# Kernel optimization log

Measured on AMD Instinct MI355X. Metric: run time of the kernel, lower is better.

The kernel has to match this reference:

```python
import jax, jax.numpy as jnp
import numpy as np

NUM_EXPERTS = 128
INPUT_DIM = 128
HIDDEN_DIM = 512
OUTPUT_DIM = 128
TOKENS_PER_EXPERT = 2048


def make_identity_experts(num_experts, input_dim, output_dim):
    # identical to the torch helper: zeros with ones on the (square) diagonal
    d = min(input_dim, output_dim)
    w = jnp.zeros((num_experts, input_dim, output_dim), dtype=jnp.float32)
    idx = jnp.arange(d)
    return w.at[:, idx, idx].set(1.0)


def setup_inputs() -> dict:
    key = jax.random.key(0)
    k_tok, = jax.random.split(key, 1)
    group_token = jax.random.normal(
        k_tok, (NUM_EXPERTS, TOKENS_PER_EXPERT, INPUT_DIM), dtype=jnp.float32)
    weights1 = make_identity_experts(NUM_EXPERTS, INPUT_DIM, HIDDEN_DIM)
    weights2 = make_identity_experts(NUM_EXPERTS, HIDDEN_DIM, OUTPUT_DIM)
    return {"group_token": group_token, "weights1": weights1, "weights2": weights2}


def reference(group_token, weights1, weights2):
    # grouped GEMM 1: per-expert [T, in] @ [in, hid]
    h = jnp.einsum('etd,edh->eth', group_token, weights1)
    # exact (erf-based) GELU, matching torch.nn.functional.gelu default
    h = jax.nn.gelu(h, approximate=False)
    # grouped GEMM 2: per-expert [T, hid] @ [hid, out]
    out = jnp.einsum('eth,eho->eto', h, weights2)
    return out
```

## Files before the change

kernel.cpp:

```cpp
#include <hip/hip_runtime.h>
#include <hip/hip_bf16.h>
#include <stdint.h>

typedef __attribute__((ext_vector_type(8))) short s8v;
typedef __attribute__((ext_vector_type(4))) float f4v;
typedef __attribute__((ext_vector_type(4))) int i4v;

#define NE   128
#define NT   2048
#define DIN  128
#define DH   512
#define DOUT 128

__device__ __forceinline__ ushort f2bf(float f) {
  uint32_t u = __float_as_uint(f);
  u += 0x7FFFu + ((u >> 16) & 1u);
  return (ushort)(u >> 16);
}

__device__ __forceinline__ float gelu_f(float x) {
  float t = 0.7978845608028654f * x * (1.0f + 0.044715f * x * x);
  float e = __expf(2.0f * t);
  float th = (e - 1.0f) / (e + 1.0f);
  return 0.5f * x * (1.0f + th);
}

__global__ __launch_bounds__(256) void transpose_cvt(
    const float* __restrict__ src, ushort* __restrict__ dst, int R, int C) {
  const int tilesR = R >> 6, tilesC = C >> 6;
  const int bid = blockIdx.x;
  const int e   = bid / (tilesR * tilesC);
  const int rem = bid % (tilesR * tilesC);
  const int tr = rem / tilesC, tc = rem % tilesC;
  const float* S = src + (size_t)e * R * C + (size_t)(tr << 6) * C + (tc << 6);
  ushort*      D = dst + (size_t)e * R * C + (size_t)(tc << 6) * R + (tr << 6);
  __shared__ float tile[64][65];
  const int tid = threadIdx.x;
#pragma unroll
  for (int it = 0; it < 4; ++it) {
    int s = (it << 8) + tid;
    int r = s >> 4, cg = (s & 15) << 2;
    float4 v = *(const float4*)(S + (size_t)r * C + cg);
    tile[r][cg + 0] = v.x; tile[r][cg + 1] = v.y;
    tile[r][cg + 2] = v.z; tile[r][cg + 3] = v.w;
  }
  __syncthreads();
#pragma unroll
  for (int it = 0; it < 4; ++it) {
    int s = (it << 8) + tid;
    int c = s >> 4, rg = (s & 15) << 2;
    ushort4 w;
    w.x = f2bf(tile[rg + 0][c]); w.y = f2bf(tile[rg + 1][c]);
    w.z = f2bf(tile[rg + 2][c]); w.w = f2bf(tile[rg + 3][c]);
    *(ushort4*)(D + (size_t)c * R + rg) = w;
  }
}

__global__ __launch_bounds__(256, 2) void moe_fused(
    const float* __restrict__ X, const ushort* __restrict__ W1t,
    const ushort* __restrict__ W2t, float* __restrict__ Out) {
  __shared__ ushort Xs[128 * 128];
  __shared__ ushort W1s[32 * 128];
  __shared__ ushort W2s[128 * 32];
  __shared__ ushort Hs[128 * 32];

  const int tid  = threadIdx.x;
  const int lane = tid & 63;
  const int wid  = tid >> 6;
  const int quad = lane >> 4;
  const int l16  = lane & 15;

  const int e    = blockIdx.x >> 4;
  const int tile = blockIdx.x & 15;

  const float*  Xe  = X   + ((size_t)e * NT + (size_t)tile * 128) * DIN;
  const ushort* W1e = W1t + (size_t)e * DH * DIN;
  const ushort* W2e = W2t + (size_t)e * DOUT * DH;
  float*        Oe  = Out + ((size_t)e * NT + (size_t)tile * 128) * DOUT;

#pragma unroll
  for (int it = 0; it < 8; ++it) {
    int s = (it << 8) + tid;
    int m = s >> 4, c = s & 15;
    const float* p = Xe + m * DIN + (c << 3);
    float4 v0 = *(const float4*)p;
    float4 v1 = *(const float4*)(p + 4);
    s8v w;
    w[0] = (short)f2bf(v0.x); w[1] = (short)f2bf(v0.y);
    w[2] = (short)f2bf(v0.z); w[3] = (short)f2bf(v0.w);
    w[4] = (short)f2bf(v1.x); w[5] = (short)f2bf(v1.y);
    w[6] = (short)f2bf(v1.z); w[7] = (short)f2bf(v1.w);
    *(s8v*)(Xs + (m << 7) + ((c ^ (m & 15)) << 3)) = w;
  }

  const f4v zero4 = {0.0f, 0.0f, 0.0f, 0.0f};
  f4v oacc[4][4];
#pragma unroll
  for (int i = 0; i < 4; ++i)
#pragma unroll
    for (int j = 0; j < 4; ++j) oacc[i][j] = zero4;

  const int w_h  = (wid >> 1) << 4;
  const int w_m1 = (wid & 1) << 6;
  const int w_m2 = (wid >> 1) << 6;
  const int w_o  = (wid & 1) << 6;

  for (int ch = 0; ch < 16; ++ch) {
    const int h0 = ch << 5;
    __syncthreads();
#pragma unroll
    for (int it = 0; it < 2; ++it) {
      int s = (it << 8) + tid;
      int r = s >> 4, c = s & 15;
      i4v v = *(const i4v*)(W1e + (size_t)(h0 + r) * DIN + (c << 3));
      *(i4v*)(W1s + (r << 7) + ((c ^ (r & 15)) << 3)) = v;
    }
#pragma unroll
    for (int it = 0; it < 2; ++it) {
      int s = (it << 8) + tid;
      int r = s >> 2, c = s & 3;
      i4v v = *(const i4v*)(W2e + (size_t)r * DH + h0 + (c << 3));
      *(i4v*)(W2s + (r << 5) + ((c ^ ((r >> 1) & 3)) << 3)) = v;
    }
    __syncthreads();

    f4v hacc[4];
    hacc[0] = zero4; hacc[1] = zero4; hacc[2] = zero4; hacc[3] = zero4;
#pragma unroll
    for (int ks = 0; ks < 4; ++ks) {
      int hl = w_h + l16;
      int ca = (ks << 2) + quad;
      s8v af = *(const s8v*)(W1s + (hl << 7) + ((ca ^ (hl & 15)) << 3));
#pragma unroll
      for (int mt = 0; mt < 4; ++mt) {
        int m = w_m1 + (mt << 4) + l16;
        s8v bf = *(const s8v*)(Xs + (m << 7) + ((ca ^ (m & 15)) << 3));
        hacc[mt] = __builtin_amdgcn_mfma_f32_16x16x32_bf16(af, bf, hacc[mt], 0, 0, 0);
      }
    }
#pragma unroll
    for (int mt = 0; mt < 4; ++mt) {
      int m  = w_m1 + (mt << 4) + l16;
      int hq = w_h + (quad << 2);
      ushort4 w;
      w.x = f2bf(gelu_f(hacc[mt][0]));
      w.y = f2bf(gelu_f(hacc[mt][1]));
      w.z = f2bf(gelu_f(hacc[mt][2]));
      w.w = f2bf(gelu_f(hacc[mt][3]));
      int cc = hq >> 3, half = (hq >> 2) & 1;
      *(ushort4*)(Hs + (m << 5) + ((cc ^ ((m >> 1) & 3)) << 3) + (half << 2)) = w;
    }
    __syncthreads();

    s8v af2[4], bf2[4];
#pragma unroll
    for (int mt = 0; mt < 4; ++mt) {
      int m = w_m2 + (mt << 4) + l16;
      af2[mt] = *(const s8v*)(Hs + (m << 5) + ((quad ^ ((m >> 1) & 3)) << 3));
    }
#pragma unroll
    for (int ot = 0; ot < 4; ++ot) {
      int o = w_o + (ot << 4) + l16;
      bf2[ot] = *(const s8v*)(W2s + (o << 5) + ((quad ^ ((o >> 1) & 3)) << 3));
    }
#pragma unroll
    for (int mt = 0; mt < 4; ++mt)
#pragma unroll
      for (int ot = 0; ot < 4; ++ot)
        oacc[mt][ot] = __builtin_amdgcn_mfma_f32_16x16x32_bf16(af2[mt], bf2[ot], oacc[mt][ot], 0, 0, 0);
  }

#pragma unroll
  for (int mt = 0; mt < 4; ++mt) {
    int mb = w_m2 + (mt << 4) + (quad << 2);
#pragma unroll
    for (int ot = 0; ot < 4; ++ot) {
      int o = w_o + (ot << 4) + l16;
      float* q = Oe + (size_t)mb * DOUT + o;
      q[0 * DOUT] = oacc[mt][ot][0];
      q[1 * DOUT] = oacc[mt][ot][1];
      q[2 * DOUT] = oacc[mt][ot][2];
      q[3 * DOUT] = oacc[mt][ot][3];
    }
  }
}

extern "C" void kernel_launch(void* const* d_in, const int* in_sizes, int n_in,
                              void* d_out, int out_size, void* d_ws, size_t ws_size,
                              hipStream_t stream) {
  const float* X  = (const float*)d_in[0];
  const float* W1 = (const float*)d_in[1];
  const float* W2 = (const float*)d_in[2];
  float* Out = (float*)d_out;

  ushort* W1t = (ushort*)d_ws;
  ushort* W2t = (ushort*)d_ws + (size_t)NE * DH * DIN;

  transpose_cvt<<<NE * (DIN / 64) * (DH / 64), 256, 0, stream>>>(W1, W1t, DIN, DH);
  transpose_cvt<<<NE * (DH / 64) * (DOUT / 64), 256, 0, stream>>>(W2, W2t, DH, DOUT);
  moe_fused<<<NE * (NT / 128), 256, 0, stream>>>(X, W1t, W2t, Out);
}
```

Before: 387.2 us.

## Pre-pack weights into MFMA fragment order and keep X and H in registers

Replaces the transpose kernels with pack kernels that write W1 and W2 already laid out in per-lane MFMA fragment order. The fused kernel now holds X fragments and the GELU output in registers, feeding the second GEMM with 16x16x16 MFMA. This removes the Xs and Hs shared buffers and one barrier per chunk. Weight chunks are double-buffered through direct global-to-LDS loads, and occupancy is raised to 3 blocks per SM. GELU becomes a sigmoid-form tanh approximation using a fast reciprocal, which adds small numerical error relative to exact erf GELU.

```diff
diff --git a/kernel.cpp b/kernel.cpp
--- a/kernel.cpp
+++ b/kernel.cpp
@@ -3,8 +3,8 @@
 #include <stdint.h>
 
 typedef __attribute__((ext_vector_type(8))) short s8v;
+typedef __attribute__((ext_vector_type(4))) short s4v;
 typedef __attribute__((ext_vector_type(4))) float f4v;
-typedef __attribute__((ext_vector_type(4))) int i4v;
 
 #define NE   128
 #define NT   2048
@@ -12,175 +12,187 @@
 #define DH   512
 #define DOUT 128
 
-__device__ __forceinline__ ushort f2bf(float f) {
-  uint32_t u = __float_as_uint(f);
-  u += 0x7FFFu + ((u >> 16) & 1u);
-  return (ushort)(u >> 16);
+#define MFMA32(a,b,c) __builtin_amdgcn_mfma_f32_16x16x32_bf16(a,b,c,0,0,0)
+#define MFMA16(a,b,c) __builtin_amdgcn_mfma_f32_16x16x16bf16_1k(a,b,c,0,0,0)
+
+#define GLOAD16(g,l) __builtin_amdgcn_global_load_lds( \
+    (const __attribute__((address_space(1))) void*)(g), \
+    (__attribute__((address_space(3))) void*)(l), 16, 0, 0)
+
+__device__ __forceinline__ __hip_bfloat162 pk2(float a, float b) {
+  float2 t; t.x = a; t.y = b;
+  return __float22bfloat162_rn(t);
+}
+
+__device__ __forceinline__ s8v pack8(float4 a, float4 b) {
+  union { s8v v; __hip_bfloat162 h[4]; } u;
+  u.h[0] = pk2(a.x, a.y); u.h[1] = pk2(a.z, a.w);
+  u.h[2] = pk2(b.x, b.y); u.h[3] = pk2(b.z, b.w);
+  return u.v;
 }
 
 __device__ __forceinline__ float gelu_f(float x) {
-  float t = 0.7978845608028654f * x * (1.0f + 0.044715f * x * x);
-  float e = __expf(2.0f * t);
-  float th = (e - 1.0f) / (e + 1.0f);
-  return 0.5f * x * (1.0f + th);
-}
-
-__global__ __launch_bounds__(256) void transpose_cvt(
-    const float* __restrict__ src, ushort* __restrict__ dst, int R, int C) {
-  const int tilesR = R >> 6, tilesC = C >> 6;
-  const int bid = blockIdx.x;
-  const int e   = bid / (tilesR * tilesC);
-  const int rem = bid % (tilesR * tilesC);
-  const int tr = rem / tilesC, tc = rem % tilesC;
-  const float* S = src + (size_t)e * R * C + (size_t)(tr << 6) * C + (tc << 6);
-  ushort*      D = dst + (size_t)e * R * C + (size_t)(tc << 6) * R + (tr << 6);
-  __shared__ float tile[64][65];
+  float x2 = x * x;
+  float p  = __builtin_fmaf(x2, 0.07135481f, 1.5957691f);
+  float e  = __expf(-x * p);
+  return x * __builtin_amdgcn_rcpf(1.0f + e);
+}
+
+__global__ __launch_bounds__(256) void pack_w1(const float* __restrict__ W1,
+                                               ushort* __restrict__ W1F) {
+  const int e = blockIdx.x >> 4, t2 = blockIdx.x & 15;
+  __shared__ float T[128][36];
   const int tid = threadIdx.x;
-#pragma unroll
-  for (int it = 0; it < 4; ++it) {
-    int s = (it << 8) + tid;
-    int r = s >> 4, cg = (s & 15) << 2;
-    float4 v = *(const float4*)(S + (size_t)r * C + cg);
-    tile[r][cg + 0] = v.x; tile[r][cg + 1] = v.y;
-    tile[r][cg + 2] = v.z; tile[r][cg + 3] = v.w;
-  }
+  const int d = tid >> 1, half = tid & 1;
+  const float* src = W1 + (size_t)e * (DIN * DH) + (size_t)d * DH + t2 * 32 + half * 16;
+  float4 v0 = *(const float4*)src;
+  float4 v1 = *(const float4*)(src + 4);
+  float4 v2 = *(const float4*)(src + 8);
+  float4 v3 = *(const float4*)(src + 12);
+  float* trow = &T[d][half * 16];
+  *(float4*)(trow + 0) = v0; *(float4*)(trow + 4)  = v1;
+  *(float4*)(trow + 8) = v2; *(float4*)(trow + 12) = v3;
   __syncthreads();
-#pragma unroll
-  for (int it = 0; it < 4; ++it) {
-    int s = (it << 8) + tid;
-    int c = s >> 4, rg = (s & 15) << 2;
-    ushort4 w;
-    w.x = f2bf(tile[rg + 0][c]); w.y = f2bf(tile[rg + 1][c]);
-    w.z = f2bf(tile[rg + 2][c]); w.w = f2bf(tile[rg + 3][c]);
-    *(ushort4*)(D + (size_t)c * R + rg) = w;
-  }
-}
-
-__global__ __launch_bounds__(256, 2) void moe_fused(
-    const float* __restrict__ X, const ushort* __restrict__ W1t,
-    const ushort* __restrict__ W2t, float* __restrict__ Out) {
-  __shared__ ushort Xs[128 * 128];
-  __shared__ ushort W1s[32 * 128];
-  __shared__ ushort W2s[128 * 32];
-  __shared__ ushort Hs[128 * 32];
+  const int lane = tid & 63, ks = tid >> 6;
+  const int q = lane >> 4, l16 = lane & 15;
+#pragma unroll
+  for (int hl = 0; hl < 2; ++hl) {
+    float g[8];
+#pragma unroll
+    for (int j = 0; j < 8; ++j) g[j] = T[ks * 32 + q * 8 + j][hl * 16 + l16];
+    float4 a; a.x = g[0]; a.y = g[1]; a.z = g[2]; a.w = g[3];
+    float4 b; b.x = g[4]; b.y = g[5]; b.z = g[6]; b.w = g[7];
+    *(s8v*)(W1F + ((((size_t)e * 32 + t2 * 2 + hl) * 4) + ks) * 512 + lane * 8) = pack8(a, b);
+  }
+}
+
+__global__ __launch_bounds__(256) void pack_w2(const float* __restrict__ W2,
+                                               ushort* __restrict__ W2F) {
+  const int e = blockIdx.x >> 5, ht = blockIdx.x & 31;
+  __shared__ float T[16][132];
+  const int tid = threadIdx.x;
+  const int h = tid >> 4, c16 = tid & 15;
+  const float* src = W2 + (size_t)e * (DH * DOUT) + (size_t)(ht * 16 + h) * DOUT + c16 * 8;
+  float4 v0 = *(const float4*)src;
+  float4 v1 = *(const float4*)(src + 4);
+  float* trow = &T[h][c16 * 8];
+  *(float4*)(trow + 0) = v0; *(float4*)(trow + 4) = v1;
+  __syncthreads();
+  const int lane = tid & 63;
+  const int q = lane >> 4, l16 = lane & 15;
+#pragma unroll
+  for (int i = 0; i < 2; ++i) {
+    int ot = (tid >> 6) + i * 4;
+    float g0 = T[4 * q + 0][ot * 16 + l16];
+    float g1 = T[4 * q + 1][ot * 16 + l16];
+    float g2 = T[4 * q + 2][ot * 16 + l16];
+    float g3 = T[4 * q + 3][ot * 16 + l16];
+    union { s4v v; __hip_bfloat162 h2[2]; } u;
+    u.h2[0] = pk2(g0, g1); u.h2[1] = pk2(g2, g3);
+    *(s4v*)(W2F + (((size_t)e * 32 + ht) * 8 + ot) * 256 + lane * 4) = u.v;
+  }
+}
+
+__global__ __launch_bounds__(256, 3) void moe_fused(
+    const float* __restrict__ X, const ushort* __restrict__ W1F,
+    const ushort* __restrict__ W2F, float* __restrict__ Out) {
+  __shared__ __align__(16) ushort W1s[2][4096];
+  __shared__ __align__(16) ushort W2s[2][4096];
 
   const int tid  = threadIdx.x;
   const int lane = tid & 63;
   const int wid  = tid >> 6;
-  const int quad = lane >> 4;
+  const int q    = lane >> 4;
   const int l16  = lane & 15;
 
   const int e    = blockIdx.x >> 4;
   const int tile = blockIdx.x & 15;
 
-  const float*  Xe  = X   + ((size_t)e * NT + (size_t)tile * 128) * DIN;
-  const ushort* W1e = W1t + (size_t)e * DH * DIN;
-  const ushort* W2e = W2t + (size_t)e * DOUT * DH;
-  float*        Oe  = Out + ((size_t)e * NT + (size_t)tile * 128) * DOUT;
-
-#pragma unroll
-  for (int it = 0; it < 8; ++it) {
-    int s = (it << 8) + tid;
-    int m = s >> 4, c = s & 15;
-    const float* p = Xe + m * DIN + (c << 3);
-    float4 v0 = *(const float4*)p;
-    float4 v1 = *(const float4*)(p + 4);
-    s8v w;
-    w[0] = (short)f2bf(v0.x); w[1] = (short)f2bf(v0.y);
-    w[2] = (short)f2bf(v0.z); w[3] = (short)f2bf(v0.w);
-    w[4] = (short)f2bf(v1.x); w[5] = (short)f2bf(v1.y);
-    w[6] = (short)f2bf(v1.z); w[7] = (short)f2bf(v1.w);
-    *(s8v*)(Xs + (m << 7) + ((c ^ (m & 15)) << 3)) = w;
+  const float* Xe  = X + ((size_t)e * NT + (size_t)tile * 128) * DIN;
+  const ushort* W1e = W1F + (size_t)e * 65536;
+  const ushort* W2e = W2F + (size_t)e * 65536;
+  float* Oe = Out + ((size_t)e * NT + (size_t)tile * 128) * DOUT;
+
+  s8v xf[2][4];
+#pragma unroll
+  for (int mt = 0; mt < 2; ++mt) {
+#pragma unroll
+    for (int ks = 0; ks < 4; ++ks) {
+      const float* p = Xe + (size_t)(wid * 32 + mt * 16 + l16) * DIN + ks * 32 + q * 8;
+      float4 v0 = *(const float4*)p;
+      float4 v1 = *(const float4*)(p + 4);
+      xf[mt][ks] = pack8(v0, v1);
+    }
   }
 
   const f4v zero4 = {0.0f, 0.0f, 0.0f, 0.0f};
-  f4v oacc[4][4];
-#pragma unroll
-  for (int i = 0; i < 4; ++i)
-#pragma unroll
-    for (int j = 0; j < 4; ++j) oacc[i][j] = zero4;
-
-  const int w_h  = (wid >> 1) << 4;
-  const int w_m1 = (wid & 1) << 6;
-  const int w_m2 = (wid >> 1) << 6;
-  const int w_o  = (wid & 1) << 6;
-
-  for (int ch = 0; ch < 16; ++ch) {
-    const int h0 = ch << 5;
+  f4v oacc[2][8];
+#pragma unroll
+  for (int mt = 0; mt < 2; ++mt)
+#pragma unroll
+    for (int ot = 0; ot < 8; ++ot) oacc[mt][ot] = zero4;
+
+  {
+    const ushort* g1 = W1e;
+    const ushort* g2 = W2e;
+#pragma unroll
+    for (int i = 0; i < 2; ++i) {
+      int u = i * 256 + tid;
+      GLOAD16(g1 + u * 8, &W1s[0][u * 8]);
+      GLOAD16(g2 + u * 8, &W2s[0][u * 8]);
+    }
+  }
+  __syncthreads();
+
+  for (int c = 0; c < 16; ++c) {
+    const int buf = c & 1;
+    if (c < 15) {
+      const ushort* g1 = W1e + (c + 1) * 4096;
+      const ushort* g2 = W2e + (c + 1) * 4096;
+#pragma unroll
+      for (int i = 0; i < 2; ++i) {
+        int u = i * 256 + tid;
+        GLOAD16(g1 + u * 8, &W1s[buf ^ 1][u * 8]);
+        GLOAD16(g2 + u * 8, &W2s[buf ^ 1][u * 8]);
+      }
+    }
+#pragma unroll
+    for (int hl = 0; hl < 2; ++hl) {
+      f4v hacc[2]; hacc[0] = zero4; hacc[1] = zero4;
+#pragma unroll
+      for (int ks = 0; ks < 4; ++ks) {
+        s8v af = *(const s8v*)&W1s[buf][(hl * 4 + ks) * 512 + lane * 8];
+        hacc[0] = MFMA32(af, xf[0][ks], hacc[0]);
+        hacc[1] = MFMA32(af, xf[1][ks], hacc[1]);
+      }
+      s4v a2[2];
+#pragma unroll
+      for (int mt = 0; mt < 2; ++mt) {
+        union { s4v v; __hip_bfloat162 h2[2]; } u;
+        u.h2[0] = pk2(gelu_f(hacc[mt][0]), gelu_f(hacc[mt][1]));
+        u.h2[1] = pk2(gelu_f(hacc[mt][2]), gelu_f(hacc[mt][3]));
+        a2[mt] = u.v;
+      }
+#pragma unroll
+      for (int ot = 0; ot < 8; ++ot) {
+        s4v bf = *(const s4v*)&W2s[buf][(hl * 8 + ot) * 256 + lane * 4];
+        oacc[0][ot] = MFMA16(a2[0], bf, oacc[0][ot]);
+        oacc[1][ot] = MFMA16(a2[1], bf, oacc[1][ot]);
+      }
+    }
     __syncthreads();
-#pragma unroll
-    for (int it = 0; it < 2; ++it) {
-      int s = (it << 8) + tid;
-      int r = s >> 4, c = s & 15;
-      i4v v = *(const i4v*)(W1e + (size_t)(h0 + r) * DIN + (c << 3));
-      *(i4v*)(W1s + (r << 7) + ((c ^ (r & 15)) << 3)) = v;
-    }
-#pragma unroll
-    for (int it = 0; it < 2; ++it) {
-      int s = (it << 8) + tid;
-      int r = s >> 2, c = s & 3;
-      i4v v = *(const i4v*)(W2e + (size_t)r * DH + h0 + (c << 3));
-      *(i4v*)(W2s + (r << 5) + ((c ^ ((r >> 1) & 3)) << 3)) = v;
-    }
-    __syncthreads();
-
-    f4v hacc[4];
-    hacc[0] = zero4; hacc[1] = zero4; hacc[2] = zero4; hacc[3] = zero4;
-#pragma unroll
-    for (int ks = 0; ks < 4; ++ks) {
-      int hl = w_h + l16;
-      int ca = (ks << 2) + quad;
-      s8v af = *(const s8v*)(W1s + (hl << 7) + ((ca ^ (hl & 15)) << 3));
-#pragma unroll
-      for (int mt = 0; mt < 4; ++mt) {
-        int m = w_m1 + (mt << 4) + l16;
-        s8v bf = *(const s8v*)(Xs + (m << 7) + ((ca ^ (m & 15)) << 3));
-        hacc[mt] = __builtin_amdgcn_mfma_f32_16x16x32_bf16(af, bf, hacc[mt], 0, 0, 0);
-      }
-    }
-#pragma unroll
-    for (int mt = 0; mt < 4; ++mt) {
-      int m  = w_m1 + (mt << 4) + l16;
-      int hq = w_h + (quad << 2);
-      ushort4 w;
-      w.x = f2bf(gelu_f(hacc[mt][0]));
-      w.y = f2bf(gelu_f(hacc[mt][1]));
-      w.z = f2bf(gelu_f(hacc[mt][2]));
-      w.w = f2bf(gelu_f(hacc[mt][3]));
-      int cc = hq >> 3, half = (hq >> 2) & 1;
-      *(ushort4*)(Hs + (m << 5) + ((cc ^ ((m >> 1) & 3)) << 3) + (half << 2)) = w;
-    }
-    __syncthreads();
-
-    s8v af2[4], bf2[4];
-#pragma unroll
-    for (int mt = 0; mt < 4; ++mt) {
-      int m = w_m2 + (mt << 4) + l16;
-      af2[mt] = *(const s8v*)(Hs + (m << 5) + ((quad ^ ((m >> 1) & 3)) << 3));
-    }
-#pragma unroll
-    for (int ot = 0; ot < 4; ++ot) {
-      int o = w_o + (ot << 4) + l16;
-      bf2[ot] = *(const s8v*)(W2s + (o << 5) + ((quad ^ ((o >> 1) & 3)) << 3));
-    }
-#pragma unroll
-    for (int mt = 0; mt < 4; ++mt)
-#pragma unroll
-      for (int ot = 0; ot < 4; ++ot)
-        oacc[mt][ot] = __builtin_amdgcn_mfma_f32_16x16x32_bf16(af2[mt], bf2[ot], oacc[mt][ot], 0, 0, 0);
-  }
-
-#pragma unroll
-  for (int mt = 0; mt < 4; ++mt) {
-    int mb = w_m2 + (mt << 4) + (quad << 2);
-#pragma unroll
-    for (int ot = 0; ot < 4; ++ot) {
-      int o = w_o + (ot << 4) + l16;
-      float* q = Oe + (size_t)mb * DOUT + o;
-      q[0 * DOUT] = oacc[mt][ot][0];
-      q[1 * DOUT] = oacc[mt][ot][1];
-      q[2 * DOUT] = oacc[mt][ot][2];
-      q[3 * DOUT] = oacc[mt][ot][3];
+  }
+
+#pragma unroll
+  for (int mt = 0; mt < 2; ++mt) {
+    const int mb = wid * 32 + mt * 16 + 4 * q;
+#pragma unroll
+    for (int ot = 0; ot < 8; ++ot) {
+      float* p = Oe + (size_t)mb * DOUT + ot * 16 + l16;
+      p[0 * DOUT] = oacc[mt][ot][0];
+      p[1 * DOUT] = oacc[mt][ot][1];
+      p[2 * DOUT] = oacc[mt][ot][2];
+      p[3 * DOUT] = oacc[mt][ot][3];
     }
   }
 }
@@ -193,10 +205,10 @@
   const float* W2 = (const float*)d_in[2];
   float* Out = (float*)d_out;
 
-  ushort* W1t = (ushort*)d_ws;
-  ushort* W2t = (ushort*)d_ws + (size_t)NE * DH * DIN;
-
-  transpose_cvt<<<NE * (DIN / 64) * (DH / 64), 256, 0, stream>>>(W1, W1t, DIN, DH);
-  transpose_cvt<<<NE * (DH / 64) * (DOUT / 64), 256, 0, stream>>>(W2, W2t, DH, DOUT);
-  moe_fused<<<NE * (NT / 128), 256, 0, stream>>>(X, W1t, W2t, Out);
-}
+  ushort* W1F = (ushort*)d_ws;
+  ushort* W2F = (ushort*)d_ws + (size_t)NE * 65536;
+
+  pack_w1<<<NE * 16, 256, 0, stream>>>(W1, W1F);
+  pack_w2<<<NE * 32, 256, 0, stream>>>(W2, W2F);
+  moe_fused<<<NE * (NT / 128), 256, 0, stream>>>(X, W1F, W2F, Out);
+}
```

Measured after the change: 336.9 us. 13.0% less time.
